# Performance work log

Hardware: AMD Instinct MI355X
Metric: run time of the kernel (lower is better)

Reference implementation:

```python
import jax, jax.numpy as jnp
import numpy as np

N = 50000   # nodes
E = 500000  # edges
B = 50      # graphs
H, D = 4, 64
NEG = 0.2   # leaky_relu slope in GATv2


def setup_inputs() -> dict:
    key = jax.random.key(0)
    ks = iter(jax.random.split(key, 40))
    rn = lambda shape, s=0.1: jax.random.normal(next(ks), shape, jnp.float32) * s
    inp = {
        'x': rn((N, 8), 1.0),
        'edge_index': jax.random.randint(next(ks), (2, E), 0, N, jnp.int64),
        'edge_attr': rn((E, 1), 1.0),
        'batch': jnp.sort(jax.random.randint(next(ks), (N,), 0, B, jnp.int64)),
        'enc_w': rn((8, 64)), 'enc_b': rn((64,)),
        'g1_wl': rn((64, 256)), 'g1_bl': rn((256,)),
        'g1_wr': rn((64, 256)), 'g1_br': rn((256,)),
        'g1_we': rn((1, 256)), 'g1_att': rn((H, D)), 'g1_bias': rn((256,)),
        'g2_wl': rn((256, 256)), 'g2_bl': rn((256,)),
        'g2_wr': rn((256, 256)), 'g2_br': rn((256,)),
        'g2_we': rn((1, 256)), 'g2_att': rn((H, D)), 'g2_bias': rn((256,)),
        'p1_w': rn((256, 128)), 'p1_b': rn((128,)),
        'ln_g': jnp.ones((128,), jnp.float32), 'ln_b': jnp.zeros((128,), jnp.float32),
        'p2_w': rn((128, 64)), 'p2_b': rn((64,)),
        'hc_w': rn((64, 1)), 'hc_b': rn((1,)),
        'hf_w': rn((64, 9)), 'hf_b': rn((9,)),
    }
    return inp


def gatv2(x, src, dst, ea, wl, bl, wr, br, we, att, bias):
    # x: [N, Fin]; src/dst: [E']; ea: [E',1]
    xl = (x @ wl + bl).reshape(N, H, D)  # source transform (lin_l)
    xr = (x @ wr + br).reshape(N, H, D)  # target transform (lin_r)
    e = (ea @ we).reshape(-1, H, D)      # edge embedding
    m = jax.nn.leaky_relu(xl[src] + xr[dst] + e, NEG)      # [E',H,D]
    logits = jnp.einsum('ehd,hd->eh', m, att)              # [E',H]
    # segment softmax over incoming edges of each target node
    lmax = jax.ops.segment_max(logits, dst, num_segments=N)
    lmax = jnp.where(jnp.isfinite(lmax), lmax, 0.0)
    ex = jnp.exp(logits - lmax[dst])
    den = jax.ops.segment_sum(ex, dst, num_segments=N)
    alpha = ex / den[dst]                                  # every node has a self-loop -> den > 0
    agg = jax.ops.segment_sum(xl[src] * alpha[:, :, None], dst, num_segments=N)
    return agg.reshape(N, H * D) + bias


def reference(x, edge_index, edge_attr, batch,
              enc_w, enc_b,
              g1_wl, g1_bl, g1_wr, g1_br, g1_we, g1_att, g1_bias,
              g2_wl, g2_bl, g2_wr, g2_br, g2_we, g2_att, g2_bias,
              p1_w, p1_b, ln_g, ln_b, p2_w, p2_b,
              hc_w, hc_b, hf_w, hf_b):
    # add self-loops once (PyG GATv2Conv default, edge_attr fill_value='mean')
    loop = jnp.arange(N, dtype=edge_index.dtype)
    src = jnp.concatenate([edge_index[0], loop])
    dst = jnp.concatenate([edge_index[1], loop])
    ea = jnp.concatenate([edge_attr,
                          jnp.broadcast_to(edge_attr.mean(0, keepdims=True), (N, 1))])

    h = jax.nn.relu(x @ enc_w + enc_b)
    h = jax.nn.relu(gatv2(h, src, dst, ea, g1_wl, g1_bl, g1_wr, g1_br, g1_we, g1_att, g1_bias))
    h = jax.nn.relu(gatv2(h, src, dst, ea, g2_wl, g2_bl, g2_wr, g2_br, g2_we, g2_att, g2_bias))

    # global mean pool over graphs
    sums = jax.ops.segment_sum(h, batch, num_segments=B)
    cnts = jax.ops.segment_sum(jnp.ones((N, 1), h.dtype), batch, num_segments=B)
    pooled = sums / jnp.maximum(cnts, 1.0)

    # post MLP: Linear -> LayerNorm -> ReLU -> (Dropout, eval=identity) -> Linear -> ReLU
    t = pooled @ p1_w + p1_b
    mu = t.mean(-1, keepdims=True)
    var = ((t - mu) ** 2).mean(-1, keepdims=True)
    t = (t - mu) / jnp.sqrt(var + 1e-5) * ln_g + ln_b
    t = jax.nn.relu(t)
    z = jax.nn.relu(t @ p2_w + p2_b)

    logit_cooling = (z @ hc_w + hc_b)[:, 0]
    logit_fatigue = z @ hf_w + hf_b
    return logit_cooling, logit_fatigue, z
```

## Files before the change

### kernel.cpp

```cpp
#include <hip/hip_runtime.h>
#include <hip/hip_bf16.h>

#define NN 50000
#define NE 500000
#define EP (NE + NN)
#define NB 50
#define NEG 0.2f
#define NBKT 196
#define CAP 3584
#define CHUNK 2048
#define NBLK1 ((EP + CHUNK - 1) / CHUNK)
#define NTILES 1563
#define GEMM_GX 392
#define SELF_FLAG (1 << 24)

#define MEAN_BLKS 256
#define ENC_BLKS 12500
#define WCONV_BLKS 640
#define ZERO_BLKS 51
#define SETUP_GRID (NBLK1 + MEAN_BLKS + ENC_BLKS + WCONV_BLKS + 1 + ZERO_BLKS)

typedef __attribute__((ext_vector_type(8))) short short8;
typedef __attribute__((ext_vector_type(4))) float f32x4;

__device__ __forceinline__ ushort f2bf(float f) {
  unsigned u = __float_as_uint(f);
  unsigned r = (u + 0x7FFFu + ((u >> 16) & 1u)) >> 16;
  return (ushort)r;
}
__device__ __forceinline__ float bf2f(ushort b) {
  return __uint_as_float(((unsigned)b) << 16);
}

__device__ __forceinline__ float exp2s(float x) {
  float r;
  asm("v_exp_f32 %0, %1\ns_nop 0" : "=v"(r) : "v"(x));
  return r;
}

__device__ __forceinline__ float row_reduce16(float x) {
  x += __int_as_float(__builtin_amdgcn_mov_dpp(__float_as_int(x), 0xB1, 0xF, 0xF, true));
  x += __int_as_float(__builtin_amdgcn_mov_dpp(__float_as_int(x), 0x4E, 0xF, 0xF, true));
  x += __int_as_float(__builtin_amdgcn_mov_dpp(__float_as_int(x), 0x124, 0xF, 0xF, true));
  x += __int_as_float(__builtin_amdgcn_mov_dpp(__float_as_int(x), 0x128, 0xF, 0xF, true));
  return x;
}

__global__ __launch_bounds__(256) void setup_kernel(
    const float* __restrict__ x, const float* __restrict__ enc_w,
    const float* __restrict__ enc_b, ushort* __restrict__ h0,
    const float* __restrict__ ea, float* __restrict__ partials,
    const int* __restrict__ ei, int* __restrict__ gcursor,
    int2* __restrict__ bucketed,
    const float* __restrict__ g1_wl, const float* __restrict__ g1_wr,
    const float* __restrict__ g2_wl, const float* __restrict__ g2_wr,
    ushort* __restrict__ w1l, ushort* __restrict__ w1r,
    ushort* __restrict__ w2l, ushort* __restrict__ w2r,
    const float* __restrict__ att1, const float* __restrict__ att2,
    float* __restrict__ a06_1, float* __restrict__ a04_1,
    float* __restrict__ a06_2, float* __restrict__ a04_2,
    float* __restrict__ zero_region) {
  __shared__ float sw[4];
  __shared__ int hist[NBKT];
  __shared__ int lbase[NBKT];
  int b = blockIdx.x, t = threadIdx.x;
  if (b < NBLK1) {
    int e0 = b * CHUNK;
    for (int i = t; i < NBKT; i += 256) hist[i] = 0;
    __syncthreads();
    int packed[8], eab[8], bkt[8];
#pragma unroll
    for (int j = 0; j < 8; j++) {
      int e = e0 + j * 256 + t;
      bool valid = e < EP;
      int src, dst, fl = 0;
      float v = 0.f;
      if (e < NE) {
        src = ei[e];
        dst = ei[NE + e];
        v = ea[e];
      } else {
        int n = valid ? (e - NE) : 0;
        src = dst = n;
        fl = SELF_FLAG;
      }
      bkt[j] = valid ? (dst >> 8) : -1;
      packed[j] = src | ((dst & 255) << 16) | fl;
      eab[j] = __float_as_int(v);
      if (valid) atomicAdd(&hist[dst >> 8], 1);
    }
    __syncthreads();
    for (int i = t; i < NBKT; i += 256)
      lbase[i] = hist[i] ? (i * CAP + atomicAdd(&gcursor[i], hist[i])) : 0;
    __syncthreads();
#pragma unroll
    for (int j = 0; j < 8; j++) {
      if (bkt[j] >= 0) {
        int pos = atomicAdd(&lbase[bkt[j]], 1);
        pos = min(pos, (bkt[j] + 1) * CAP - 1);
        bucketed[pos] = make_int2(packed[j], eab[j]);
      }
    }
    return;
  }
  b -= NBLK1;
  if (b < MEAN_BLKS) {
    int idx = b * 256 + t;
    float v = 0.f;
    for (int i = idx; i < NE; i += 65536) v += ea[i];
    for (int off = 1; off < 64; off <<= 1) v += __shfl_xor(v, off, 64);
    if ((t & 63) == 0) sw[t >> 6] = v;
    __syncthreads();
    if (t == 0) partials[b] = sw[0] + sw[1] + sw[2] + sw[3];
    return;
  }
  b -= MEAN_BLKS;
  if (b < ENC_BLKS) {
    int i = b * 256 + t;
    int n = i >> 6, j = i & 63;
    float acc = enc_b[j];
#pragma unroll
    for (int k = 0; k < 8; k++) acc += x[n * 8 + k] * enc_w[k * 64 + j];
    h0[i] = f2bf(fmaxf(acc, 0.f));
    return;
  }
  b -= ENC_BLKS;
  if (b < WCONV_BLKS) {
    if (b < 128) {
      int sec = b >> 6;
      const float* W = sec ? g1_wr : g1_wl;
      ushort* Wt = sec ? w1r : w1l;
      int i = (b & 63) * 256 + t;
      int n = i >> 6, k = i & 63;
      Wt[i] = f2bf(W[(size_t)k * 256 + n]);
    } else {
      int bb = b - 128;
      int sec = bb >> 8;
      const float* W = sec ? g2_wr : g2_wl;
      ushort* Wt = sec ? w2r : w2l;
      int i = (bb & 255) * 256 + t;
      int n = i >> 8, k = i & 255;
      Wt[i] = f2bf(W[(size_t)k * 256 + n]);
    }
    return;
  }
  b -= WCONV_BLKS;
  if (b == 0) {
    const float L2E = 1.44269504f;
    float v1 = att1[t], v2 = att2[t];
    a06_1[t] = 0.6f * L2E * v1;
    a04_1[t] = 0.4f * L2E * v1;
    a06_2[t] = 0.6f * L2E * v2;
    a04_2[t] = 0.4f * L2E * v2;
    return;
  }
  b -= 1;
  {
    int i = b * 256 + t;
    if (i < NB * 256 + NB) zero_region[i] = 0.f;
  }
}

__global__ __launch_bounds__(256) void bucket_sort_kernel(const int* __restrict__ gcursor,
                                                          const float* __restrict__ partials,
                                                          const int2* __restrict__ bucketed,
                                                          int2* __restrict__ sedge,
                                                          int* __restrict__ offsets,
                                                          int* __restrict__ counts) {
  __shared__ int2 stage[CAP];
  __shared__ int hist[256], scn[256], cur[256];
  __shared__ float sw[4];
  int b = blockIdx.x, t = threadIdx.x;
  float pv = partials[t];
  for (int off = 1; off < 64; off <<= 1) pv += __shfl_xor(pv, off, 64);
  if ((t & 63) == 0) sw[t >> 6] = pv;
  hist[t] = 0;
  __syncthreads();
  int meanb = __float_as_int((sw[0] + sw[1] + sw[2] + sw[3]) * (1.0f / NE));
  int base = b * CAP;
  int nb = min(gcursor[b], CAP - 16);
  for (int i = t; i < nb; i += 256) {
    int2 s = bucketed[base + i];
    if (s.x & SELF_FLAG) s.y = meanb;
    stage[i] = s;
  }
  __syncthreads();
  if (t < 16) {
    int2 pv2 = make_int2((stage[0].x & 0xFFFF) << 9, stage[0].y);
    sedge[base + nb + t] = pv2;
  }
  for (int i = t; i < nb; i += 256) atomicAdd(&hist[(stage[i].x >> 16) & 255], 1);
  __syncthreads();
  int v = hist[t];
  scn[t] = v;
  __syncthreads();
  for (int off = 1; off < 256; off <<= 1) {
    int add = (t >= off) ? scn[t - off] : 0;
    __syncthreads();
    scn[t] += add;
    __syncthreads();
  }
  int excl = scn[t] - v;
  cur[t] = excl;
  __syncthreads();
  for (int i = t; i < nb; i += 256) {
    int dl = (stage[i].x >> 16) & 255;
    int p = atomicAdd(&cur[dl], 1);
    sedge[base + p] = make_int2((stage[i].x & 0xFFFF) << 9, stage[i].y);
  }
  int d = b * 256 + t;
  if (d < NN) {
    offsets[d] = base + excl;
    counts[d] = v;
  }
}

template <int K>
__global__ __launch_bounds__(256) void dual_linear_pb(const ushort* __restrict__ A,
                                                      const ushort* __restrict__ Wl,
                                                      const ushort* __restrict__ Wr,
                                                      const float* __restrict__ bl,
                                                      const float* __restrict__ br,
                                                      ushort* __restrict__ xl,
                                                      ushort* __restrict__ xr) {
  __shared__ ushort lt[32][272];
  int wave = threadIdx.x >> 6, lane = threadIdx.x & 63;
  int lr = lane & 15;
  int kb = (lane >> 4) * 8;
  const ushort* W = blockIdx.y ? Wr : Wl;
  const float* bias = blockIdx.y ? br : bl;
  ushort* O = blockIdx.y ? xr : xl;
  const int c0 = wave * 64;
  const ushort* pb = W + (size_t)(c0 + lr) * K + kb;
  int tid = threadIdx.x;
  int cb = (tid & 31) * 8;

  for (int t = blockIdx.x; t < NTILES; t += GEMM_GX) {
    int r = t * 32;
    int ra0 = min(r + lr, NN - 1);
    int ra1 = min(r + 16 + lr, NN - 1);
    const ushort* pa0 = A + (size_t)ra0 * K + kb;
    const ushort* pa1 = A + (size_t)ra1 * K + kb;
    f32x4 acc[2][4];
#pragma unroll
    for (int fr = 0; fr < 2; fr++)
#pragma unroll
      for (int fc = 0; fc < 4; fc++) acc[fr][fc] = (f32x4){0.f, 0.f, 0.f, 0.f};
#pragma unroll
    for (int kc = 0; kc < K; kc += 64) {
      short8 a00 = *(const short8*)(pa0 + kc);
      short8 a01 = *(const short8*)(pa0 + kc + 32);
      short8 a10 = *(const short8*)(pa1 + kc);
      short8 a11 = *(const short8*)(pa1 + kc + 32);
      short8 b0[4], b1[4];
#pragma unroll
      for (int fc = 0; fc < 4; fc++) {
        b0[fc] = *(const short8*)(pb + (size_t)fc * 16 * K + kc);
        b1[fc] = *(const short8*)(pb + (size_t)fc * 16 * K + kc + 32);
      }
#pragma unroll
      for (int fc = 0; fc < 4; fc++) {
        acc[0][fc] = __builtin_amdgcn_mfma_f32_16x16x32_bf16(a00, b0[fc], acc[0][fc], 0, 0, 0);
        acc[1][fc] = __builtin_amdgcn_mfma_f32_16x16x32_bf16(a10, b0[fc], acc[1][fc], 0, 0, 0);
      }
#pragma unroll
      for (int fc = 0; fc < 4; fc++) {
        acc[0][fc] = __builtin_amdgcn_mfma_f32_16x16x32_bf16(a01, b1[fc], acc[0][fc], 0, 0, 0);
        acc[1][fc] = __builtin_amdgcn_mfma_f32_16x16x32_bf16(a11, b1[fc], acc[1][fc], 0, 0, 0);
      }
    }
#pragma unroll
    for (int fc = 0; fc < 4; fc++) {
      int c = c0 + fc * 16 + lr;
      float bv = bias[c];
#pragma unroll
      for (int fr = 0; fr < 2; fr++) {
#pragma unroll
        for (int j = 0; j < 4; j++) {
          int row = fr * 16 + (lane >> 4) * 4 + j;
          int cs = c ^ (((row >> 2) & 3) << 4);
          lt[row][cs] = f2bf(acc[fr][fc][j] + bv);
        }
      }
    }
    __syncthreads();
#pragma unroll
    for (int it = 0; it < 4; it++) {
      int rl = (tid >> 5) + it * 8;
      int row = r + rl;
      if (row < NN) {
        int cs = cb ^ (((rl >> 2) & 3) << 4);
        short8 v = *(const short8*)&lt[rl][cs];
        *(short8*)(O + (size_t)row * 256 + cb) = v;
      }
    }
    __syncthreads();
  }
}

__global__ __launch_bounds__(256) void gat_fused_kernel(const int* __restrict__ offsets,
                                                        const int* __restrict__ counts,
                                                        const int2* __restrict__ sedge,
                                                        const ushort* __restrict__ xl,
                                                        const ushort* __restrict__ xr,
                                                        const float* __restrict__ we,
                                                        const float* __restrict__ a06p,
                                                        const float* __restrict__ a04p,
                                                        const float* __restrict__ bias,
                                                        ushort* __restrict__ hb) {
  int w = threadIdx.x >> 6, lane = threadIdx.x & 63;
  int d = blockIdx.x * 4 + w;
  if (d >= NN) return;
  int off = offsets[d], cnt = counts[d];
  const int c4 = lane * 4;
  ushort4 xru = *(const ushort4*)(xr + (size_t)d * 256 + c4);
  const float4 xr4 = {bf2f(xru.x), bf2f(xru.y), bf2f(xru.z), bf2f(xru.w)};
  const float4 we4 = *(const float4*)(we + c4);
  const float4 a06 = *(const float4*)(a06p + c4);
  const float4 a04 = *(const float4*)(a04p + c4);
  float4 acc = {0.f, 0.f, 0.f, 0.f};
  float den = 0.f;
  const int2* pe = sedge + off;
  const char* xlc = (const char*)xl + (size_t)c4 * 2;
  int2 e0 = pe[0], e1 = pe[1], e2 = pe[2], e3 = pe[3];
  ushort4 xu0 = *(const ushort4*)(xlc + (size_t)(unsigned)e0.x);
  ushort4 xu1 = *(const ushort4*)(xlc + (size_t)(unsigned)e1.x);
  ushort4 xu2 = *(const ushort4*)(xlc + (size_t)(unsigned)e2.x);
  ushort4 xu3 = *(const ushort4*)(xlc + (size_t)(unsigned)e3.x);
  int2 f0 = pe[4], f1 = pe[5], f2 = pe[6], f3 = pe[7];
  ushort4 yu0 = *(const ushort4*)(xlc + (size_t)(unsigned)f0.x);
  ushort4 yu1 = *(const ushort4*)(xlc + (size_t)(unsigned)f1.x);
  ushort4 yu2 = *(const ushort4*)(xlc + (size_t)(unsigned)f2.x);
  ushort4 yu3 = *(const ushort4*)(xlc + (size_t)(unsigned)f3.x);
#pragma unroll 2
  for (int i = 0; i < cnt; i += 4) {
    float ce0 = __int_as_float(e0.y), ce1 = __int_as_float(e1.y);
    float ce2 = __int_as_float(e2.y), ce3 = __int_as_float(e3.y);
    float4 x0 = {bf2f(xu0.x), bf2f(xu0.y), bf2f(xu0.z), bf2f(xu0.w)};
    float4 x1 = {bf2f(xu1.x), bf2f(xu1.y), bf2f(xu1.z), bf2f(xu1.w)};
    float4 x2 = {bf2f(xu2.x), bf2f(xu2.y), bf2f(xu2.z), bf2f(xu2.w)};
    float4 x3 = {bf2f(xu3.x), bf2f(xu3.y), bf2f(xu3.z), bf2f(xu3.w)};
    e0 = f0; e1 = f1; e2 = f2; e3 = f3;
    xu0 = yu0; xu1 = yu1; xu2 = yu2; xu3 = yu3;
    f0 = pe[i + 8]; f1 = pe[i + 9]; f2 = pe[i + 10]; f3 = pe[i + 11];
    yu0 = *(const ushort4*)(xlc + (size_t)(unsigned)f0.x);
    yu1 = *(const ushort4*)(xlc + (size_t)(unsigned)f1.x);
    yu2 = *(const ushort4*)(xlc + (size_t)(unsigned)f2.x);
    yu3 = *(const ushort4*)(xlc + (size_t)(unsigned)f3.x);
    float v0, v1, v2, v3;
    float p0, p1, p2, p3;
    v0 = x0.x + fmaf(ce0, we4.x, xr4.x);
    v1 = x0.y + fmaf(ce0, we4.y, xr4.y);
    v2 = x0.z + fmaf(ce0, we4.z, xr4.z);
    v3 = x0.w + fmaf(ce0, we4.w, xr4.w);
    p0 = fmaf(a06.x, v0, a04.x * fabsf(v0));
    p0 = fmaf(a06.y, v1, fmaf(a04.y, fabsf(v1), p0));
    p0 = fmaf(a06.z, v2, fmaf(a04.z, fabsf(v2), p0));
    p0 = fmaf(a06.w, v3, fmaf(a04.w, fabsf(v3), p0));
    v0 = x1.x + fmaf(ce1, we4.x, xr4.x);
    v1 = x1.y + fmaf(ce1, we4.y, xr4.y);
    v2 = x1.z + fmaf(ce1, we4.z, xr4.z);
    v3 = x1.w + fmaf(ce1, we4.w, xr4.w);
    p1 = fmaf(a06.x, v0, a04.x * fabsf(v0));
    p1 = fmaf(a06.y, v1, fmaf(a04.y, fabsf(v1), p1));
    p1 = fmaf(a06.z, v2, fmaf(a04.z, fabsf(v2), p1));
    p1 = fmaf(a06.w, v3, fmaf(a04.w, fabsf(v3), p1));
    v0 = x2.x + fmaf(ce2, we4.x, xr4.x);
    v1 = x2.y + fmaf(ce2, we4.y, xr4.y);
    v2 = x2.z + fmaf(ce2, we4.z, xr4.z);
    v3 = x2.w + fmaf(ce2, we4.w, xr4.w);
    p2 = fmaf(a06.x, v0, a04.x * fabsf(v0));
    p2 = fmaf(a06.y, v1, fmaf(a04.y, fabsf(v1), p2));
    p2 = fmaf(a06.z, v2, fmaf(a04.z, fabsf(v2), p2));
    p2 = fmaf(a06.w, v3, fmaf(a04.w, fabsf(v3), p2));
    v0 = x3.x + fmaf(ce3, we4.x, xr4.x);
    v1 = x3.y + fmaf(ce3, we4.y, xr4.y);
    v2 = x3.z + fmaf(ce3, we4.z, xr4.z);
    v3 = x3.w + fmaf(ce3, we4.w, xr4.w);
    p3 = fmaf(a06.x, v0, a04.x * fabsf(v0));
    p3 = fmaf(a06.y, v1, fmaf(a04.y, fabsf(v1), p3));
    p3 = fmaf(a06.z, v2, fmaf(a04.z, fabsf(v2), p3));
    p3 = fmaf(a06.w, v3, fmaf(a04.w, fabsf(v3), p3));
    p0 = row_reduce16(p0);
    p1 = row_reduce16(p1);
    p2 = row_reduce16(p2);
    p3 = row_reduce16(p3);
    float ex0 = exp2s(fminf(p0, 120.f));
    float ex1 = exp2s(fminf(p1, 120.f));
    float ex2 = exp2s(fminf(p2, 120.f));
    float ex3 = exp2s(fminf(p3, 120.f));
    ex1 = (i + 1 < cnt) ? ex1 : 0.f;
    ex2 = (i + 2 < cnt) ? ex2 : 0.f;
    ex3 = (i + 3 < cnt) ? ex3 : 0.f;
    den += (ex0 + ex1) + (ex2 + ex3);
    acc.x = fmaf(x0.x, ex0, fmaf(x1.x, ex1, fmaf(x2.x, ex2, fmaf(x3.x, ex3, acc.x))));
    acc.y = fmaf(x0.y, ex0, fmaf(x1.y, ex1, fmaf(x2.y, ex2, fmaf(x3.y, ex3, acc.y))));
    acc.z = fmaf(x0.z, ex0, fmaf(x1.z, ex1, fmaf(x2.z, ex2, fmaf(x3.z, ex3, acc.z))));
    acc.w = fmaf(x0.w, ex0, fmaf(x1.w, ex1, fmaf(x2.w, ex2, fmaf(x3.w, ex3, acc.w))));
  }
  const float4 b4 = *(const float4*)(bias + c4);
  float inv = 1.f / den;
  ushort4 o;
  o.x = f2bf(fmaxf(fmaf(acc.x, inv, b4.x), 0.f));
  o.y = f2bf(fmaxf(fmaf(acc.y, inv, b4.y), 0.f));
  o.z = f2bf(fmaxf(fmaf(acc.z, inv, b4.z), 0.f));
  o.w = f2bf(fmaxf(fmaf(acc.w, inv, b4.w), 0.f));
  *(ushort4*)(hb + (size_t)d * 256 + c4) = o;
}

__global__ __launch_bounds__(256) void pool_kernel(const ushort* __restrict__ h,
                                                   const int* __restrict__ batch,
                                                   float* __restrict__ sums,
                                                   float* __restrict__ cnts) {
  __shared__ int sb[128];
  int n0 = blockIdx.x * 128;
  int j = threadIdx.x;
  int count = min(128, NN - n0);
  if (count <= 0) return;
  for (int t = threadIdx.x; t < count; t += 256) sb[t] = batch[n0 + t];
  __syncthreads();
  float acc = 0.f;
  int run = 0;
  int cur = sb[0];
  for (int i = 0; i < count; ++i) {
    int b = sb[i];
    if (b != cur) {
      atomicAdd(&sums[(size_t)cur * 256 + j], acc);
      if (j == 0) atomicAdd(&cnts[cur], (float)run);
      acc = 0.f;
      run = 0;
      cur = b;
    }
    acc += bf2f(h[(size_t)(n0 + i) * 256 + j]);
    run++;
  }
  atomicAdd(&sums[(size_t)cur * 256 + j], acc);
  if (j == 0) atomicAdd(&cnts[cur], (float)run);
}

__global__ __launch_bounds__(128) void head_kernel(const float* __restrict__ sums,
                                                   const float* __restrict__ cnts,
                                                   const float* __restrict__ p1_w,
                                                   const float* __restrict__ p1_b,
                                                   const float* __restrict__ ln_g,
                                                   const float* __restrict__ ln_b,
                                                   const float* __restrict__ p2_w,
                                                   const float* __restrict__ p2_b,
                                                   const float* __restrict__ hc_w,
                                                   const float* __restrict__ hc_b,
                                                   const float* __restrict__ hf_w,
                                                   const float* __restrict__ hf_b,
                                                   float* __restrict__ out) {
  int g = blockIdx.x;
  int j = threadIdx.x;
  __shared__ float sp[256], st[128], sz[64];
  float cnt = fmaxf(cnts[g], 1.0f);
  for (int t = j; t < 256; t += 128) sp[t] = sums[(size_t)g * 256 + t] / cnt;
  __syncthreads();
  float acc = p1_b[j];
  for (int k = 0; k < 256; k++) acc += sp[k] * p1_w[(size_t)k * 128 + j];
  st[j] = acc;
  __syncthreads();
  float mu = 0.f;
  for (int k = 0; k < 128; k++) mu += st[k];
  mu *= (1.f / 128.f);
  float var = 0.f;
  for (int k = 0; k < 128; k++) {
    float d = st[k] - mu;
    var += d * d;
  }
  var *= (1.f / 128.f);
  float tj = (acc - mu) * rsqrtf(var + 1e-5f) * ln_g[j] + ln_b[j];
  tj = fmaxf(tj, 0.f);
  __syncthreads();
  st[j] = tj;
  __syncthreads();
  if (j < 64) {
    float z = p2_b[j];
    for (int k = 0; k < 128; k++) z += st[k] * p2_w[(size_t)k * 64 + j];
    z = fmaxf(z, 0.f);
    sz[j] = z;
    out[500 + (size_t)g * 64 + j] = z;
  }
  __syncthreads();
  if (j == 0) {
    float c = hc_b[0];
    for (int k = 0; k < 64; k++) c += sz[k] * hc_w[k];
    out[g] = c;
  }
  if (j >= 1 && j < 10) {
    int f = j - 1;
    float v = hf_b[f];
    for (int k = 0; k < 64; k++) v += sz[k] * hf_w[(size_t)k * 9 + f];
    out[50 + (size_t)g * 9 + f] = v;
  }
}

extern "C" void kernel_launch(void* const* d_in, const int* in_sizes, int n_in,
                              void* d_out, int out_size, void* d_ws, size_t ws_size,
                              hipStream_t stream) {
  const float* x = (const float*)d_in[0];
  const int* ei = (const int*)d_in[1];
  const float* ea = (const float*)d_in[2];
  const int* batch = (const int*)d_in[3];
  const float* enc_w = (const float*)d_in[4];
  const float* enc_b = (const float*)d_in[5];
  const float* g1_wl = (const float*)d_in[6];
  const float* g1_bl = (const float*)d_in[7];
  const float* g1_wr = (const float*)d_in[8];
  const float* g1_br = (const float*)d_in[9];
  const float* g1_we = (const float*)d_in[10];
  const float* g1_att = (const float*)d_in[11];
  const float* g1_bias = (const float*)d_in[12];
  const float* g2_wl = (const float*)d_in[13];
  const float* g2_bl = (const float*)d_in[14];
  const float* g2_wr = (const float*)d_in[15];
  const float* g2_br = (const float*)d_in[16];
  const float* g2_we = (const float*)d_in[17];
  const float* g2_att = (const float*)d_in[18];
  const float* g2_bias = (const float*)d_in[19];
  const float* p1_w = (const float*)d_in[20];
  const float* p1_b = (const float*)d_in[21];
  const float* ln_g = (const float*)d_in[22];
  const float* ln_b = (const float*)d_in[23];
  const float* p2_w = (const float*)d_in[24];
  const float* p2_b = (const float*)d_in[25];
  const float* hc_w = (const float*)d_in[26];
  const float* hc_b = (const float*)d_in[27];
  const float* hf_w = (const float*)d_in[28];
  const float* hf_b = (const float*)d_in[29];
  float* out = (float*)d_out;

  ushort* xlb = (ushort*)d_ws;
  ushort* xrb = xlb + (size_t)NN * 256;
  ushort* hb = xrb + (size_t)NN * 256;
  ushort* h0b = hb + (size_t)NN * 256;
  ushort* w1l = h0b + (size_t)NN * 64;
  ushort* w1r = w1l + 256 * 64;
  ushort* w2l = w1r + 256 * 64;
  ushort* w2r = w2l + 256 * 256;
  int2* bucketed = (int2*)(w2r + 256 * 256);
  int2* sedge = bucketed + (size_t)NBKT * CAP;
  int* gcursor = (int*)(sedge + (size_t)NBKT * CAP);
  int* counts = gcursor + NBKT;
  int* offsets = counts + NN;
  float* sums = (float*)(offsets + NN);
  float* cnts = sums + (size_t)NB * 256;
  float* partials = cnts + NB;
  float* a06_1 = partials + 256;
  float* a04_1 = a06_1 + 256;
  float* a06_2 = a04_1 + 256;
  float* a04_2 = a06_2 + 256;

  hipMemsetAsync(gcursor, 0, NBKT * sizeof(int), stream);

  setup_kernel<<<SETUP_GRID, 256, 0, stream>>>(
      x, enc_w, enc_b, h0b, ea, partials, ei, gcursor, bucketed,
      g1_wl, g1_wr, g2_wl, g2_wr, w1l, w1r, w2l, w2r,
      g1_att, g2_att, a06_1, a04_1, a06_2, a04_2, sums);

  bucket_sort_kernel<<<NBKT, 256, 0, stream>>>(gcursor, partials, bucketed, sedge,
                                               offsets, counts);

  const dim3 gemmGrid(GEMM_GX, 2);
  const int nGatBlocks = (NN + 3) / 4;

  dual_linear_pb<64><<<gemmGrid, 256, 0, stream>>>(h0b, w1l, w1r, g1_bl, g1_br, xlb, xrb);
  gat_fused_kernel<<<nGatBlocks, 256, 0, stream>>>(offsets, counts, sedge, xlb, xrb,
                                                   g1_we, a06_1, a04_1, g1_bias, hb);

  dual_linear_pb<256><<<gemmGrid, 256, 0, stream>>>(hb, w2l, w2r, g2_bl, g2_br, xlb, xrb);
  gat_fused_kernel<<<nGatBlocks, 256, 0, stream>>>(offsets, counts, sedge, xlb, xrb,
                                                   g2_we, a06_2, a04_2, g2_bias, hb);

  pool_kernel<<<(NN + 127) / 128, 256, 0, stream>>>(hb, batch, sums, cnts);
  head_kernel<<<NB, 128, 0, stream>>>(sums, cnts, p1_w, p1_b, ln_g, ln_b, p2_w, p2_b,
                                      hc_w, hc_b, hf_w, hf_b, out);
}
```

Measured before the change: 251.5 us.

## Fuse bucket sort into first GEMM launch as extra blocks

The bucket sort kernel is merged into the first dual_linear launch by adding NBKT extra blocks along x that run the sort while the remaining blocks compute the layer-1 projections. Both paths share one shared-memory buffer, sized to the larger of the two uses. This removes one kernel launch and its serialization gap, and lets the sort overlap with the GEMM. In exchange, GEMM blocks now reserve the larger shared-memory footprint, which may lower occupancy, and the blockIdx.y=1 copies of the sort blocks exit right away.

Result: faster. 242.9 us (-3.4%).

```diff
diff --git a/kernel.cpp b/kernel.cpp
--- a/kernel.cpp
+++ b/kernel.cpp
@@ -13,6 +13,7 @@
 #define NTILES 1563
 #define GEMM_GX 392
 #define SELF_FLAG (1 << 24)
+#define SMEM_BYTES 31760
 
 #define MEAN_BLKS 256
 #define ENC_BLKS 12500
@@ -161,70 +162,71 @@
   }
 }
 
-__global__ __launch_bounds__(256) void bucket_sort_kernel(const int* __restrict__ gcursor,
-                                                          const float* __restrict__ partials,
-                                                          const int2* __restrict__ bucketed,
-                                                          int2* __restrict__ sedge,
-                                                          int* __restrict__ offsets,
-                                                          int* __restrict__ counts) {
-  __shared__ int2 stage[CAP];
-  __shared__ int hist[256], scn[256], cur[256];
-  __shared__ float sw[4];
-  int b = blockIdx.x, t = threadIdx.x;
-  float pv = partials[t];
-  for (int off = 1; off < 64; off <<= 1) pv += __shfl_xor(pv, off, 64);
-  if ((t & 63) == 0) sw[t >> 6] = pv;
-  hist[t] = 0;
-  __syncthreads();
-  int meanb = __float_as_int((sw[0] + sw[1] + sw[2] + sw[3]) * (1.0f / NE));
-  int base = b * CAP;
-  int nb = min(gcursor[b], CAP - 16);
-  for (int i = t; i < nb; i += 256) {
-    int2 s = bucketed[base + i];
-    if (s.x & SELF_FLAG) s.y = meanb;
-    stage[i] = s;
-  }
-  __syncthreads();
-  if (t < 16) {
-    int2 pv2 = make_int2((stage[0].x & 0xFFFF) << 9, stage[0].y);
-    sedge[base + nb + t] = pv2;
-  }
-  for (int i = t; i < nb; i += 256) atomicAdd(&hist[(stage[i].x >> 16) & 255], 1);
-  __syncthreads();
-  int v = hist[t];
-  scn[t] = v;
-  __syncthreads();
-  for (int off = 1; off < 256; off <<= 1) {
-    int add = (t >= off) ? scn[t - off] : 0;
-    __syncthreads();
-    scn[t] += add;
-    __syncthreads();
-  }
-  int excl = scn[t] - v;
-  cur[t] = excl;
-  __syncthreads();
-  for (int i = t; i < nb; i += 256) {
-    int dl = (stage[i].x >> 16) & 255;
-    int p = atomicAdd(&cur[dl], 1);
-    sedge[base + p] = make_int2((stage[i].x & 0xFFFF) << 9, stage[i].y);
-  }
-  int d = b * 256 + t;
-  if (d < NN) {
-    offsets[d] = base + excl;
-    counts[d] = v;
-  }
-}
-
-template <int K>
-__global__ __launch_bounds__(256) void dual_linear_pb(const ushort* __restrict__ A,
-                                                      const ushort* __restrict__ Wl,
-                                                      const ushort* __restrict__ Wr,
-                                                      const float* __restrict__ bl,
-                                                      const float* __restrict__ br,
-                                                      ushort* __restrict__ xl,
-                                                      ushort* __restrict__ xr) {
-  __shared__ ushort lt[32][272];
-  int wave = threadIdx.x >> 6, lane = threadIdx.x & 63;
+template <int K, bool WITH_SORT>
+__global__ __launch_bounds__(256) void dual_linear_pb(
+    const ushort* __restrict__ A, const ushort* __restrict__ Wl,
+    const ushort* __restrict__ Wr, const float* __restrict__ bl,
+    const float* __restrict__ br, ushort* __restrict__ xl,
+    ushort* __restrict__ xr,
+    const int* __restrict__ gcursor, const float* __restrict__ partials,
+    const int2* __restrict__ bucketed, int2* __restrict__ sedge,
+    int* __restrict__ offsets, int* __restrict__ counts) {
+  __shared__ __align__(16) char smem[SMEM_BYTES];
+  int t = threadIdx.x;
+  if (WITH_SORT && blockIdx.x >= GEMM_GX) {
+    if (blockIdx.y != 0) return;
+    int2* stage = (int2*)smem;
+    int* hist = (int*)(smem + CAP * 8);
+    int* scn = hist + 256;
+    int* cur = scn + 256;
+    float* sw = (float*)(cur + 256);
+    int b = blockIdx.x - GEMM_GX;
+    float pv = partials[t];
+    for (int off = 1; off < 64; off <<= 1) pv += __shfl_xor(pv, off, 64);
+    if ((t & 63) == 0) sw[t >> 6] = pv;
+    hist[t] = 0;
+    __syncthreads();
+    int meanb = __float_as_int((sw[0] + sw[1] + sw[2] + sw[3]) * (1.0f / NE));
+    int base = b * CAP;
+    int nb = min(gcursor[b], CAP - 16);
+    for (int i = t; i < nb; i += 256) {
+      int2 s = bucketed[base + i];
+      if (s.x & SELF_FLAG) s.y = meanb;
+      stage[i] = s;
+    }
+    __syncthreads();
+    if (t < 16) {
+      int2 pv2 = make_int2((stage[0].x & 0xFFFF) << 9, stage[0].y);
+      sedge[base + nb + t] = pv2;
+    }
+    for (int i = t; i < nb; i += 256) atomicAdd(&hist[(stage[i].x >> 16) & 255], 1);
+    __syncthreads();
+    int v = hist[t];
+    scn[t] = v;
+    __syncthreads();
+    for (int off = 1; off < 256; off <<= 1) {
+      int add = (t >= off) ? scn[t - off] : 0;
+      __syncthreads();
+      scn[t] += add;
+      __syncthreads();
+    }
+    int excl = scn[t] - v;
+    cur[t] = excl;
+    __syncthreads();
+    for (int i = t; i < nb; i += 256) {
+      int dl = (stage[i].x >> 16) & 255;
+      int p = atomicAdd(&cur[dl], 1);
+      sedge[base + p] = make_int2((stage[i].x & 0xFFFF) << 9, stage[i].y);
+    }
+    int d = b * 256 + t;
+    if (d < NN) {
+      offsets[d] = base + excl;
+      counts[d] = v;
+    }
+    return;
+  }
+  ushort(*lt)[272] = reinterpret_cast<ushort(*)[272]>(smem);
+  int wave = t >> 6, lane = t & 63;
   int lr = lane & 15;
   int kb = (lane >> 4) * 8;
   const ushort* W = blockIdx.y ? Wr : Wl;
@@ -232,11 +234,10 @@
   ushort* O = blockIdx.y ? xr : xl;
   const int c0 = wave * 64;
   const ushort* pb = W + (size_t)(c0 + lr) * K + kb;
-  int tid = threadIdx.x;
-  int cb = (tid & 31) * 8;
-
-  for (int t = blockIdx.x; t < NTILES; t += GEMM_GX) {
-    int r = t * 32;
+  int cb = (t & 31) * 8;
+
+  for (int tt = blockIdx.x; tt < NTILES; tt += GEMM_GX) {
+    int r = tt * 32;
     int ra0 = min(r + lr, NN - 1);
     int ra1 = min(r + 16 + lr, NN - 1);
     const ushort* pa0 = A + (size_t)ra0 * K + kb;
@@ -286,7 +287,7 @@
     __syncthreads();
 #pragma unroll
     for (int it = 0; it < 4; it++) {
-      int rl = (tid >> 5) + it * 8;
+      int rl = (t >> 5) + it * 8;
       int row = r + rl;
       if (row < NN) {
         int cs = cb ^ (((rl >> 2) & 3) << 4);
@@ -559,17 +560,19 @@
       g1_wl, g1_wr, g2_wl, g2_wr, w1l, w1r, w2l, w2r,
       g1_att, g2_att, a06_1, a04_1, a06_2, a04_2, sums);
 
-  bucket_sort_kernel<<<NBKT, 256, 0, stream>>>(gcursor, partials, bucketed, sedge,
-                                               offsets, counts);
-
-  const dim3 gemmGrid(GEMM_GX, 2);
   const int nGatBlocks = (NN + 3) / 4;
 
-  dual_linear_pb<64><<<gemmGrid, 256, 0, stream>>>(h0b, w1l, w1r, g1_bl, g1_br, xlb, xrb);
+  dim3 g64(GEMM_GX + NBKT, 2);
+  dual_linear_pb<64, true><<<g64, 256, 0, stream>>>(
+      h0b, w1l, w1r, g1_bl, g1_br, xlb, xrb,
+      gcursor, partials, bucketed, sedge, offsets, counts);
   gat_fused_kernel<<<nGatBlocks, 256, 0, stream>>>(offsets, counts, sedge, xlb, xrb,
                                                    g1_we, a06_1, a04_1, g1_bias, hb);
 
-  dual_linear_pb<256><<<gemmGrid, 256, 0, stream>>>(hb, w2l, w2r, g2_bl, g2_br, xlb, xrb);
+  dim3 g256(GEMM_GX, 2);
+  dual_linear_pb<256, false><<<g256, 256, 0, stream>>>(
+      hb, w2l, w2r, g2_bl, g2_br, xlb, xrb,
+      gcursor, partials, bucketed, sedge, offsets, counts);
   gat_fused_kernel<<<nGatBlocks, 256, 0, stream>>>(offsets, counts, sedge, xlb, xrb,
                                                    g2_we, a06_2, a04_2, g2_bias, hb);
 
```
